# Performance work log

Measured on AMD Instinct MI355X. Metric: run time of the kernel, lower is better.

## Reference

```python
import jax, jax.numpy as jnp
import numpy as np

N_NODES = 100000
D_IN = 128
D_OUT = 128
SHAPES = {"r1": 1, "r2": 2, "r3": 3}
N_EDGES = {"r1": 400000, "r2": 300000, "r3": 200000}


def setup_inputs() -> dict:
    key = jax.random.key(0)
    ks = jax.random.split(key, 10)
    inp = {
        "x": jax.random.normal(ks[0], (N_NODES, D_IN), dtype=jnp.float32),
        "A_r1": jax.random.normal(ks[1], (D_IN * 1, D_OUT), dtype=jnp.float32) * 0.05,
        "A_r2": jax.random.normal(ks[2], (D_IN * 2, D_OUT), dtype=jnp.float32) * 0.05,
        "A_r3": jax.random.normal(ks[3], (D_IN * 3, D_OUT), dtype=jnp.float32) * 0.05,
        "C_w": jax.random.normal(ks[4], (D_IN, D_OUT), dtype=jnp.float32) * 0.05,
        "C_b": jax.random.normal(ks[5], (D_OUT,), dtype=jnp.float32) * 0.05,
    }
    for j, (name, shape) in enumerate(SHAPES.items()):
        n = N_EDGES[name] * shape
        inp[f"ei_{name}"] = jax.random.randint(ks[6 + j], (2, n), 0, N_NODES, dtype=jnp.int64)
    return inp


def _edge_type_agg(x, edge_indices, A, shape):
    # edge_indices: [2, n_edges*shape]; row0 = sources, row1 reshaped -> dest per hyperedge
    dest = edge_indices[1].reshape(-1, shape)[:, 0]          # [n_edges]
    gathered = x[edge_indices[0]].reshape(-1, shape * x.shape[1])  # [n_edges, shape*D_IN]
    msg = gathered @ A                                        # [n_edges, D_OUT]
    # 1/count(dest) normalization (torch.unique counts == per-type in-degree)
    deg = jax.ops.segment_sum(jnp.ones_like(dest, dtype=msg.dtype), dest, num_segments=x.shape[0])
    msg = msg / deg[dest][:, None]
    return jax.ops.segment_sum(msg, dest, num_segments=x.shape[0])  # scatter_add


def reference(x, ei_r1, ei_r2, ei_r3, A_r1, A_r2, A_r3, C_w, C_b):
    agg = (_edge_type_agg(x, ei_r1, A_r1, 1)
           + _edge_type_agg(x, ei_r2, A_r2, 2)
           + _edge_type_agg(x, ei_r3, A_r3, 3))
    return x @ C_w + C_b + agg
```

## Files before the change

### kernel.cpp

```cpp
#include <hip/hip_runtime.h>

#define N_NODES 100000
#define D 128
#define NND 12800000L

typedef unsigned short u16;
typedef short s16x8 __attribute__((ext_vector_type(8)));
typedef float f32x4 __attribute__((ext_vector_type(4)));


#define ENTS_OFF 2004160L
#define AT_OFF   15604224L
#define Y_OFF    15833600L

__device__ __forceinline__ u16 f2b(float f) {
    union { float f; unsigned u; } v; v.f = f;
    unsigned r = (v.u + 0x7FFFu + ((v.u >> 16) & 1u)) >> 16;
    return (u16)r;
}
__device__ __forceinline__ float blo(unsigned w) { return __uint_as_float(w << 16); }
__device__ __forceinline__ float bhi(unsigned w) { return __uint_as_float(w & 0xFFFF0000u); }


__global__ __launch_bounds__(256) void init_kernel(
    const float* __restrict__ A1, const float* __restrict__ A2,
    const float* __restrict__ A3, const float* __restrict__ Cw,
    u16* __restrict__ ATb, int* __restrict__ deg) {
    int b = blockIdx.x, t = threadIdx.x;
    if (b < 293) {
        int i0 = (b * 256 + t) * 4;
#pragma unroll
        for (int r = 0; r < 4; r++)
            if (i0 + r < 300000) deg[i0 + r] = 0;
        return;
    }
    int mb = b - 293;
    int m = mb >> 6;
    int idx = (mb & 63) * 256 + t;
    int n = idx >> 7, kk = idx & 127;
    const float* src; int srow;
    if (m == 0)      { src = A1; srow = kk; }
    else if (m < 3)  { src = A2; srow = (m - 1) * 128 + kk; }
    else if (m < 6)  { src = A3; srow = (m - 3) * 128 + kk; }
    else             { src = Cw; srow = kk; }
    ATb[m * 16384 + n * 128 + kk] = f2b(src[(long)srow * 128 + n]);
}


__global__ __launch_bounds__(256) void deg_all(
    const int* __restrict__ e1, const int* __restrict__ e2, const int* __restrict__ e3,
    int ne1, int ne2, int ne3, int* __restrict__ deg) {
    int g = blockIdx.x * 256 + threadIdx.x;
    if (g < ne1) {
        atomicAdd(&deg[e1[ne1 + g]], 1);
    } else if (g < ne1 + ne2) {
        int e = g - ne1;
        atomicAdd(&deg[N_NODES + e2[ne2 * 2 + e * 2]], 1);
    } else if (g < ne1 + ne2 + ne3) {
        int e = g - ne1 - ne2;
        atomicAdd(&deg[2 * N_NODES + e3[ne3 * 3 + e * 3]], 1);
    }
}

__device__ __forceinline__ int ucnt(const int* deg, int d) {
    return 1 + deg[d] + 2 * deg[N_NODES + d] + 3 * deg[2 * N_NODES + d];
}


__global__ __launch_bounds__(256) void scan_reduce_u(const int* __restrict__ deg,
                                                     int* __restrict__ bsums, int n) {
    __shared__ int s[256];
    int t = threadIdx.x;
    int base = blockIdx.x * 1024 + t * 4;
    int loc = 0;
#pragma unroll
    for (int r = 0; r < 4; r++) {
        int idx = base + r;
        if (idx < n) loc += ucnt(deg, idx);
    }
    s[t] = loc;
    for (int off = 128; off > 0; off >>= 1) {
        __syncthreads();
        if (t < off) s[t] += s[t + off];
    }
    if (t == 0) bsums[blockIdx.x] = s[0];
}

__global__ __launch_bounds__(512) void scan_tops(const int* __restrict__ bsums,
                                                 int* __restrict__ boffs,
                                                 int* __restrict__ offs, int nb, int n) {
    __shared__ int s[512];
    int t = threadIdx.x;
    int v = (t < nb) ? bsums[t] : 0;
    s[t] = v;
    for (int off = 1; off < 512; off <<= 1) {
        __syncthreads();
        int x = (t >= off) ? s[t - off] : 0;
        __syncthreads();
        s[t] += x;
    }
    if (t < nb) boffs[t] = s[t] - v;
    if (t == nb - 1) offs[n] = s[t];
}

__global__ __launch_bounds__(256) void scan_final_u(
    const int* __restrict__ deg, const int* __restrict__ boffs,
    int* __restrict__ offs, int* __restrict__ cursor, int2* __restrict__ ents, int n) {
    __shared__ int s[256];
    int t = threadIdx.x;
    int base = blockIdx.x * 1024 + t * 4;
    int v[4], p[4];
#pragma unroll
    for (int r = 0; r < 4; r++) {
        int idx = base + r;
        v[r] = (idx < n) ? ucnt(deg, idx) : 0;
    }
    p[0] = 0; p[1] = v[0]; p[2] = v[0] + v[1]; p[3] = v[0] + v[1] + v[2];
    int tsum = p[3] + v[3];
    s[t] = tsum;
    for (int off = 1; off < 256; off <<= 1) {
        __syncthreads();
        int x = (t >= off) ? s[t - off] : 0;
        __syncthreads();
        s[t] += x;
    }
    int texcl = s[t] - tsum + boffs[blockIdx.x];
#pragma unroll
    for (int r = 0; r < 4; r++) {
        int idx = base + r;
        if (idx < n) {
            int val = texcl + p[r];
            offs[idx] = val;
            cursor[idx] = val + 1;
            ents[val] = make_int2(6 * N_NODES + idx, __float_as_int(1.0f));
        }
    }
}


__global__ __launch_bounds__(256) void scatter_all(
    const int* __restrict__ e1, const int* __restrict__ e2, const int* __restrict__ e3,
    int ne1, int ne2, int ne3, const int* __restrict__ deg,
    int* __restrict__ cursor, int2* __restrict__ ents) {
    int g = blockIdx.x * 256 + threadIdx.x;
    if (g < ne1) {
        int dest = e1[ne1 + g];
        float sc = 1.0f / (float)deg[dest];
        int pos = atomicAdd(&cursor[dest], 1);
        ents[pos] = make_int2(e1[g], __float_as_int(sc));
    } else if (g < ne1 + ne2) {
        int e = g - ne1;
        int dest = e2[ne2 * 2 + e * 2];
        float sc = 1.0f / (float)deg[N_NODES + dest];
        int pos = atomicAdd(&cursor[dest], 2);
        ents[pos]     = make_int2(1 * N_NODES + e2[e * 2],     __float_as_int(sc));
        ents[pos + 1] = make_int2(2 * N_NODES + e2[e * 2 + 1], __float_as_int(sc));
    } else if (g < ne1 + ne2 + ne3) {
        int e = g - ne1 - ne2;
        int dest = e3[ne3 * 3 + e * 3];
        float sc = 1.0f / (float)deg[2 * N_NODES + dest];
        int pos = atomicAdd(&cursor[dest], 3);
#pragma unroll
        for (int s = 0; s < 3; s++)
            ents[pos + s] = make_int2((3 + s) * N_NODES + e3[e * 3 + s], __float_as_int(sc));
    }
}


__global__ __launch_bounds__(256) void gemm_all(
    const float* __restrict__ x, const u16* __restrict__ AT, u16* __restrict__ Y) {
    __shared__ float smemf[64 * 132];
    typedef u16 XsT[64][40];
    XsT* Xs = reinterpret_cast<XsT*>(smemf);

    const int t = threadIdx.x;
    const int d0 = blockIdx.x * 64;

#pragma unroll
    for (int i = 0; i < 8; i++) {
        int f = i * 256 + t;
        int row = f >> 5;
        int k4 = f & 31;
        int rs = d0 + row < N_NODES ? d0 + row : N_NODES - 1;
        float4 v = *(const float4*)&x[(long)rs * D + k4 * 4];
        int chunk = k4 >> 3, kk = (k4 & 7) * 4;
        u16* p = &Xs[chunk][row][kk];
        p[0] = f2b(v.x); p[1] = f2b(v.y); p[2] = f2b(v.z); p[3] = f2b(v.w);
    }
    __syncthreads();

    const int lane = t & 63, wv = t >> 6;
    const int nbase = wv * 32, quad = lane >> 4, lrow = lane & 15;

    s16x8 afrag[4][4];
#pragma unroll
    for (int mi = 0; mi < 4; mi++)
#pragma unroll
        for (int c = 0; c < 4; c++)
            afrag[mi][c] = *(const s16x8*)&Xs[c][mi * 16 + lrow][quad * 8];

    for (int w = 0; w < 7; w++) {
        const u16* B = AT + w * 16384;
        s16x8 bfrag[2][4];
#pragma unroll
        for (int ni = 0; ni < 2; ni++)
#pragma unroll
            for (int c = 0; c < 4; c++)
                bfrag[ni][c] = *(const s16x8*)(B + (long)(nbase + ni * 16 + lrow) * 128 +
                                               c * 32 + quad * 8);
        f32x4 acc[4][2];
#pragma unroll
        for (int mi = 0; mi < 4; mi++)
#pragma unroll
            for (int ni = 0; ni < 2; ni++) acc[mi][ni] = (f32x4)(0.0f);
#pragma unroll
        for (int c = 0; c < 4; c++)
#pragma unroll
            for (int mi = 0; mi < 4; mi++)
#pragma unroll
                for (int ni = 0; ni < 2; ni++)
                    acc[mi][ni] = __builtin_amdgcn_mfma_f32_16x16x32_bf16(
                        afrag[mi][c], bfrag[ni][c], acc[mi][ni], 0, 0, 0);

        __syncthreads();
#pragma unroll
        for (int mi = 0; mi < 4; mi++)
#pragma unroll
            for (int ni = 0; ni < 2; ni++)
#pragma unroll
                for (int reg = 0; reg < 4; reg++) {
                    int row = mi * 16 + quad * 4 + reg;
                    int col = nbase + ni * 16 + lrow;
                    smemf[row * 132 + col] = acc[mi][ni][reg];
                }
        __syncthreads();
        u16* Yw = Y + (long)w * NND;
#pragma unroll
        for (int i = 0; i < 8; i++) {
            int f = i * 256 + t;
            int row = f >> 5;
            int col = (f & 31) * 4;
            if (d0 + row < N_NODES) {
                float4 v = *(const float4*)&smemf[row * 132 + col];
                unsigned o0 = (unsigned)f2b(v.x) | ((unsigned)f2b(v.y) << 16);
                unsigned o1 = (unsigned)f2b(v.z) | ((unsigned)f2b(v.w) << 16);
                uint2 o = make_uint2(o0, o1);
                *(uint2*)(Yw + (long)(d0 + row) * D + col) = o;
            }
        }
        __syncthreads();
    }
}


__global__ __launch_bounds__(256) void gather_all(
    const u16* __restrict__ Y, const int2* __restrict__ ents,
    const int* __restrict__ offs, const float* __restrict__ Cb,
    float* __restrict__ out) {
    const int lane = threadIdx.x & 63;
    const int wv = __builtin_amdgcn_readfirstlane(threadIdx.x >> 6);
    int wid = blockIdx.x * 4 + wv;
    const int nw = gridDim.x * 4;
    const float cb0 = Cb[lane * 2];
    const float cb1 = Cb[lane * 2 + 1];

    for (int d = wid; d < N_NODES; d += nw) {
        int lo = offs[d];
        int hi = offs[d + 1];
        float a0 = 0.0f, a1 = 0.0f;
        for (int p = lo; p < hi; p += 8) {
            int2 e[8];
#pragma unroll
            for (int i = 0; i < 8; i++) {
                int q = p + i;
                e[i] = ents[q < hi ? q : hi - 1];
            }
            unsigned w[8];
#pragma unroll
            for (int i = 0; i < 8; i++)
                w[i] = *(const unsigned*)(Y + (long)e[i].x * D + lane * 2);
#pragma unroll
            for (int i = 0; i < 8; i++) {
                float s = (p + i < hi) ? __int_as_float(e[i].y) : 0.0f;
                a0 = fmaf(s, blo(w[i]), a0);
                a1 = fmaf(s, bhi(w[i]), a1);
            }
        }
        *(float2*)&out[(long)d * D + lane * 2] = make_float2(a0 + cb0, a1 + cb1);
    }
}


extern "C" void kernel_launch(void* const* d_in, const int* in_sizes, int n_in,
                              void* d_out, int out_size, void* d_ws, size_t ws_size,
                              hipStream_t stream) {
    const float* x  = (const float*)d_in[0];
    const float* A1 = (const float*)d_in[1];
    const float* A2 = (const float*)d_in[2];
    const float* A3 = (const float*)d_in[3];
    const float* Cw = (const float*)d_in[4];
    const float* Cb = (const float*)d_in[5];
    const int* e1 = (const int*)d_in[6];
    const int* e2 = (const int*)d_in[7];
    const int* e3 = (const int*)d_in[8];
    float* out = (float*)d_out;

    int* ws = (int*)d_ws;
    int* deg    = ws;
    int* offs   = ws + 300000;
    int* cursor = ws + 400001;
    int* bsums  = ws + 500001;
    int* boffs  = ws + 500513;
    int2* ents  = (int2*)((char*)d_ws + ENTS_OFF);
    u16* ATb    = (u16*)((char*)d_ws + AT_OFF);
    u16* Y      = (u16*)((char*)d_ws + Y_OFF);

    const int NE1 = in_sizes[6] / 2;
    const int NE2 = in_sizes[7] / (2 * 2);
    const int NE3 = in_sizes[8] / (2 * 3);
    const int NET = NE1 + NE2 + NE3;
    const int n = N_NODES;
    const int NB = (n + 1023) / 1024;

    init_kernel<<<293 + 448, 256, 0, stream>>>(A1, A2, A3, Cw, ATb, deg);
    deg_all<<<(NET + 255) / 256, 256, 0, stream>>>(e1, e2, e3, NE1, NE2, NE3, deg);
    scan_reduce_u<<<NB, 256, 0, stream>>>(deg, bsums, n);
    scan_tops<<<1, 512, 0, stream>>>(bsums, boffs, offs, NB, n);
    scan_final_u<<<NB, 256, 0, stream>>>(deg, boffs, offs, cursor, ents, n);
    scatter_all<<<(NET + 255) / 256, 256, 0, stream>>>(e1, e2, e3, NE1, NE2, NE3,
                                                       deg, cursor, ents);
    gemm_all<<<(N_NODES + 63) / 64, 256, 0, stream>>>(x, ATb, Y);
    gather_all<<<2048, 256, 0, stream>>>(Y, ents, offs, Cb, out);
}
```

Before: 354.8 us.

## Aggregate raw features before projection, then run a single fused GEMM

Uses linearity to swap the order of work: neighbour features are gathered and averaged per destination and per hyperedge slot into a 7x128 bf16 staging row per node, and a single GEMM then projects the concatenated row to the output and adds the bias. Before, seven 128-wide bf16 projections were written to global memory and gathered back. Edge entries shrink to plain source ints grouped by type and slot, and normalisation is done once per node instead of per edge. The cost is a larger K=896 GEMM that reloads its A tile from global memory for each slice, plus an extra 896-wide bf16 staging buffer.

```diff
diff --git a/kernel.cpp b/kernel.cpp
--- a/kernel.cpp
+++ b/kernel.cpp
@@ -2,30 +2,33 @@
 
 #define N_NODES 100000
 #define D 128
-#define NND 12800000L
 
 typedef unsigned short u16;
 typedef short s16x8 __attribute__((ext_vector_type(8)));
 typedef float f32x4 __attribute__((ext_vector_type(4)));
 
 
-#define ENTS_OFF 2004160L
-#define AT_OFF   15604224L
-#define Y_OFF    15833600L
+#define ENTS_OFF 2804224L
+#define AT_OFF   9204224L
+#define G_OFF    9433600L
 
 __device__ __forceinline__ u16 f2b(float f) {
     union { float f; unsigned u; } v; v.f = f;
     unsigned r = (v.u + 0x7FFFu + ((v.u >> 16) & 1u)) >> 16;
     return (u16)r;
 }
+__device__ __forceinline__ unsigned pk(float lo, float hi) {
+    return (unsigned)f2b(lo) | ((unsigned)f2b(hi) << 16);
+}
 __device__ __forceinline__ float blo(unsigned w) { return __uint_as_float(w << 16); }
 __device__ __forceinline__ float bhi(unsigned w) { return __uint_as_float(w & 0xFFFF0000u); }
 
 
 __global__ __launch_bounds__(256) void init_kernel(
+    const float* __restrict__ x,
     const float* __restrict__ A1, const float* __restrict__ A2,
     const float* __restrict__ A3, const float* __restrict__ Cw,
-    u16* __restrict__ ATb, int* __restrict__ deg) {
+    u16* __restrict__ ATb, u16* __restrict__ G, int* __restrict__ deg) {
     int b = blockIdx.x, t = threadIdx.x;
     if (b < 293) {
         int i0 = (b * 256 + t) * 4;
@@ -34,16 +37,28 @@
             if (i0 + r < 300000) deg[i0 + r] = 0;
         return;
     }
-    int mb = b - 293;
-    int m = mb >> 6;
-    int idx = (mb & 63) * 256 + t;
-    int n = idx >> 7, kk = idx & 127;
-    const float* src; int srow;
-    if (m == 0)      { src = A1; srow = kk; }
-    else if (m < 3)  { src = A2; srow = (m - 1) * 128 + kk; }
-    else if (m < 6)  { src = A3; srow = (m - 3) * 128 + kk; }
-    else             { src = Cw; srow = kk; }
-    ATb[m * 16384 + n * 128 + kk] = f2b(src[(long)srow * 128 + n]);
+    if (b < 741) {
+        int mb = b - 293;
+        int m = mb >> 6;
+        int idx = (mb & 63) * 256 + t;
+        int n = idx >> 7, kk = idx & 127;
+        const float* src; int srow;
+        if (m == 0)      { src = A1; srow = kk; }
+        else if (m < 3)  { src = A2; srow = (m - 1) * 128 + kk; }
+        else if (m < 6)  { src = A3; srow = (m - 3) * 128 + kk; }
+        else             { src = Cw; srow = kk; }
+        ATb[m * 16384 + n * 128 + kk] = f2b(src[(long)srow * 128 + n]);
+        return;
+    }
+    int f = (b - 741) * 256 + t;
+    int node = f >> 4, j = f & 15;
+    const float* xr = x + (long)node * 128 + j * 8;
+    float4 v0 = *(const float4*)xr;
+    float4 v1 = *(const float4*)(xr + 4);
+    uint4 o;
+    o.x = pk(v0.x, v0.y); o.y = pk(v0.z, v0.w);
+    o.z = pk(v1.x, v1.y); o.w = pk(v1.z, v1.w);
+    *(uint4*)(G + (long)node * 896 + 768 + j * 8) = o;
 }
 
 
@@ -63,7 +78,7 @@
 }
 
 __device__ __forceinline__ int ucnt(const int* deg, int d) {
-    return 1 + deg[d] + 2 * deg[N_NODES + d] + 3 * deg[2 * N_NODES + d];
+    return deg[d] + 2 * deg[N_NODES + d] + 3 * deg[2 * N_NODES + d];
 }
 
 
@@ -105,7 +120,7 @@
 
 __global__ __launch_bounds__(256) void scan_final_u(
     const int* __restrict__ deg, const int* __restrict__ boffs,
-    int* __restrict__ offs, int* __restrict__ cursor, int2* __restrict__ ents, int n) {
+    int* __restrict__ offs, int* __restrict__ cursor, int n) {
     __shared__ int s[256];
     int t = threadIdx.x;
     int base = blockIdx.x * 1024 + t * 4;
@@ -131,8 +146,10 @@
         if (idx < n) {
             int val = texcl + p[r];
             offs[idx] = val;
-            cursor[idx] = val + 1;
-            ents[val] = make_int2(6 * N_NODES + idx, __float_as_int(1.0f));
+            int c1 = deg[idx], c2 = deg[N_NODES + idx];
+            cursor[idx] = val;
+            cursor[N_NODES + idx] = val + c1;
+            cursor[2 * N_NODES + idx] = val + c1 + 2 * c2;
         }
     }
 }
@@ -141,152 +158,189 @@
 __global__ __launch_bounds__(256) void scatter_all(
     const int* __restrict__ e1, const int* __restrict__ e2, const int* __restrict__ e3,
     int ne1, int ne2, int ne3, const int* __restrict__ deg,
-    int* __restrict__ cursor, int2* __restrict__ ents) {
+    int* __restrict__ cursor, int* __restrict__ ents) {
     int g = blockIdx.x * 256 + threadIdx.x;
     if (g < ne1) {
         int dest = e1[ne1 + g];
-        float sc = 1.0f / (float)deg[dest];
         int pos = atomicAdd(&cursor[dest], 1);
-        ents[pos] = make_int2(e1[g], __float_as_int(sc));
+        ents[pos] = e1[g];
     } else if (g < ne1 + ne2) {
         int e = g - ne1;
         int dest = e2[ne2 * 2 + e * 2];
-        float sc = 1.0f / (float)deg[N_NODES + dest];
-        int pos = atomicAdd(&cursor[dest], 2);
-        ents[pos]     = make_int2(1 * N_NODES + e2[e * 2],     __float_as_int(sc));
-        ents[pos + 1] = make_int2(2 * N_NODES + e2[e * 2 + 1], __float_as_int(sc));
+        int c2 = deg[N_NODES + dest];
+        int pos = atomicAdd(&cursor[N_NODES + dest], 1);
+        ents[pos]      = e2[e * 2];
+        ents[pos + c2] = e2[e * 2 + 1];
     } else if (g < ne1 + ne2 + ne3) {
         int e = g - ne1 - ne2;
         int dest = e3[ne3 * 3 + e * 3];
-        float sc = 1.0f / (float)deg[2 * N_NODES + dest];
-        int pos = atomicAdd(&cursor[dest], 3);
-#pragma unroll
-        for (int s = 0; s < 3; s++)
-            ents[pos + s] = make_int2((3 + s) * N_NODES + e3[e * 3 + s], __float_as_int(sc));
-    }
-}
-
-
-__global__ __launch_bounds__(256) void gemm_all(
-    const float* __restrict__ x, const u16* __restrict__ AT, u16* __restrict__ Y) {
-    __shared__ float smemf[64 * 132];
+        int c3 = deg[2 * N_NODES + dest];
+        int pos = atomicAdd(&cursor[2 * N_NODES + dest], 1);
+        ents[pos]          = e3[e * 3];
+        ents[pos + c3]     = e3[e * 3 + 1];
+        ents[pos + 2 * c3] = e3[e * 3 + 2];
+    }
+}
+
+
+__global__ __launch_bounds__(256) void agg_all(
+    u16* __restrict__ G, const int* __restrict__ ents,
+    const int* __restrict__ offs, const int* __restrict__ deg) {
+    const int lane = threadIdx.x & 63;
+    const int wv = threadIdx.x >> 6;
+    int wid = blockIdx.x * 4 + wv;
+    const int nw = gridDim.x * 4;
+    const int col = lane * 2;
+
+    for (int d = wid; d < N_NODES; d += nw) {
+        const int lo = offs[d];
+        const int c1 = deg[d], c2 = deg[N_NODES + d], c3 = deg[2 * N_NODES + d];
+        float a0l = 0, a0h = 0, a1l = 0, a1h = 0, a2l = 0, a2h = 0;
+        float a3l = 0, a3h = 0, a4l = 0, a4h = 0, a5l = 0, a5h = 0;
+
+        for (int p = 0; p < c1; p += 4) {
+            unsigned w[4]; float m[4];
+#pragma unroll
+            for (int i = 0; i < 4; i++) {
+                int q = (p + i < c1) ? p + i : c1 - 1;
+                int src = ents[lo + q];
+                w[i] = *(const unsigned*)(G + (long)src * 896 + 768 + col);
+                m[i] = (p + i < c1) ? 1.0f : 0.0f;
+            }
+#pragma unroll
+            for (int i = 0; i < 4; i++) {
+                a0l = fmaf(m[i], blo(w[i]), a0l);
+                a0h = fmaf(m[i], bhi(w[i]), a0h);
+            }
+        }
+        const int o1 = lo + c1;
+        for (int p = 0; p < c2; p += 4) {
+            unsigned wa[4], wb[4]; float m[4];
+#pragma unroll
+            for (int i = 0; i < 4; i++) {
+                int q = (p + i < c2) ? p + i : c2 - 1;
+                int sa = ents[o1 + q];
+                int sb = ents[o1 + q + c2];
+                wa[i] = *(const unsigned*)(G + (long)sa * 896 + 768 + col);
+                wb[i] = *(const unsigned*)(G + (long)sb * 896 + 768 + col);
+                m[i] = (p + i < c2) ? 1.0f : 0.0f;
+            }
+#pragma unroll
+            for (int i = 0; i < 4; i++) {
+                a1l = fmaf(m[i], blo(wa[i]), a1l); a1h = fmaf(m[i], bhi(wa[i]), a1h);
+                a2l = fmaf(m[i], blo(wb[i]), a2l); a2h = fmaf(m[i], bhi(wb[i]), a2h);
+            }
+        }
+        const int o3 = o1 + 2 * c2;
+        for (int p = 0; p < c3; p += 4) {
+            unsigned wa[4], wb[4], wc[4]; float m[4];
+#pragma unroll
+            for (int i = 0; i < 4; i++) {
+                int q = (p + i < c3) ? p + i : c3 - 1;
+                int sa = ents[o3 + q];
+                int sb = ents[o3 + q + c3];
+                int sc = ents[o3 + q + 2 * c3];
+                wa[i] = *(const unsigned*)(G + (long)sa * 896 + 768 + col);
+                wb[i] = *(const unsigned*)(G + (long)sb * 896 + 768 + col);
+                wc[i] = *(const unsigned*)(G + (long)sc * 896 + 768 + col);
+                m[i] = (p + i < c3) ? 1.0f : 0.0f;
+            }
+#pragma unroll
+            for (int i = 0; i < 4; i++) {
+                a3l = fmaf(m[i], blo(wa[i]), a3l); a3h = fmaf(m[i], bhi(wa[i]), a3h);
+                a4l = fmaf(m[i], blo(wb[i]), a4l); a4h = fmaf(m[i], bhi(wb[i]), a4h);
+                a5l = fmaf(m[i], blo(wc[i]), a5l); a5h = fmaf(m[i], bhi(wc[i]), a5h);
+            }
+        }
+        const float i1 = c1 ? 1.0f / (float)c1 : 0.0f;
+        const float i2 = c2 ? 1.0f / (float)c2 : 0.0f;
+        const float i3 = c3 ? 1.0f / (float)c3 : 0.0f;
+        u16* gd = G + (long)d * 896 + col;
+        *(unsigned*)(gd)       = pk(a0l * i1, a0h * i1);
+        *(unsigned*)(gd + 128) = pk(a1l * i2, a1h * i2);
+        *(unsigned*)(gd + 256) = pk(a2l * i2, a2h * i2);
+        *(unsigned*)(gd + 384) = pk(a3l * i3, a3h * i3);
+        *(unsigned*)(gd + 512) = pk(a4l * i3, a4h * i3);
+        *(unsigned*)(gd + 640) = pk(a5l * i3, a5h * i3);
+    }
+}
+
+
+__global__ __launch_bounds__(256) void gemm_out(
+    const u16* __restrict__ G, const u16* __restrict__ AT,
+    const float* __restrict__ Cb, float* __restrict__ out) {
+    __shared__ __align__(16) float smemf[64 * 132];
     typedef u16 XsT[64][40];
     XsT* Xs = reinterpret_cast<XsT*>(smemf);
 
     const int t = threadIdx.x;
     const int d0 = blockIdx.x * 64;
-
+    const int lane = t & 63, wv = t >> 6;
+    const int nbase = wv * 32, quad = lane >> 4, lrow = lane & 15;
+
+    f32x4 acc[4][2];
+#pragma unroll
+    for (int mi = 0; mi < 4; mi++)
+#pragma unroll
+        for (int ni = 0; ni < 2; ni++) acc[mi][ni] = (f32x4)(0.0f);
+
+    for (int s = 0; s < 7; s++) {
+#pragma unroll
+        for (int i = 0; i < 4; i++) {
+            int f = i * 256 + t;
+            int row = f >> 4, k8 = f & 15;
+            long rs = (d0 + row < N_NODES) ? d0 + row : N_NODES - 1;
+            uint4 v = *(const uint4*)(G + rs * 896 + s * 128 + k8 * 8);
+            *(uint4*)&Xs[k8 >> 2][row][(k8 & 3) * 8] = v;
+        }
+        __syncthreads();
+        const u16* B = AT + s * 16384;
+        s16x8 bfrag[2][4];
+#pragma unroll
+        for (int ni = 0; ni < 2; ni++)
+#pragma unroll
+            for (int c = 0; c < 4; c++)
+                bfrag[ni][c] = *(const s16x8*)(B + (nbase + ni * 16 + lrow) * 128 +
+                                               c * 32 + quad * 8);
+        s16x8 afrag[4][4];
+#pragma unroll
+        for (int mi = 0; mi < 4; mi++)
+#pragma unroll
+            for (int c = 0; c < 4; c++)
+                afrag[mi][c] = *(const s16x8*)&Xs[c][mi * 16 + lrow][quad * 8];
+#pragma unroll
+        for (int c = 0; c < 4; c++)
+#pragma unroll
+            for (int mi = 0; mi < 4; mi++)
+#pragma unroll
+                for (int ni = 0; ni < 2; ni++)
+                    acc[mi][ni] = __builtin_amdgcn_mfma_f32_16x16x32_bf16(
+                        afrag[mi][c], bfrag[ni][c], acc[mi][ni], 0, 0, 0);
+        __syncthreads();
+    }
+
+#pragma unroll
+    for (int mi = 0; mi < 4; mi++)
+#pragma unroll
+        for (int ni = 0; ni < 2; ni++)
+#pragma unroll
+            for (int reg = 0; reg < 4; reg++) {
+                int row = mi * 16 + quad * 4 + reg;
+                int colq = nbase + ni * 16 + lrow;
+                smemf[row * 132 + colq] = acc[mi][ni][reg];
+            }
+    __syncthreads();
 #pragma unroll
     for (int i = 0; i < 8; i++) {
         int f = i * 256 + t;
         int row = f >> 5;
-        int k4 = f & 31;
-        int rs = d0 + row < N_NODES ? d0 + row : N_NODES - 1;
-        float4 v = *(const float4*)&x[(long)rs * D + k4 * 4];
-        int chunk = k4 >> 3, kk = (k4 & 7) * 4;
-        u16* p = &Xs[chunk][row][kk];
-        p[0] = f2b(v.x); p[1] = f2b(v.y); p[2] = f2b(v.z); p[3] = f2b(v.w);
-    }
-    __syncthreads();
-
-    const int lane = t & 63, wv = t >> 6;
-    const int nbase = wv * 32, quad = lane >> 4, lrow = lane & 15;
-
-    s16x8 afrag[4][4];
-#pragma unroll
-    for (int mi = 0; mi < 4; mi++)
-#pragma unroll
-        for (int c = 0; c < 4; c++)
-            afrag[mi][c] = *(const s16x8*)&Xs[c][mi * 16 + lrow][quad * 8];
-
-    for (int w = 0; w < 7; w++) {
-        const u16* B = AT + w * 16384;
-        s16x8 bfrag[2][4];
-#pragma unroll
-        for (int ni = 0; ni < 2; ni++)
-#pragma unroll
-            for (int c = 0; c < 4; c++)
-                bfrag[ni][c] = *(const s16x8*)(B + (long)(nbase + ni * 16 + lrow) * 128 +
-                                               c * 32 + quad * 8);
-        f32x4 acc[4][2];
-#pragma unroll
-        for (int mi = 0; mi < 4; mi++)
-#pragma unroll
-            for (int ni = 0; ni < 2; ni++) acc[mi][ni] = (f32x4)(0.0f);
-#pragma unroll
-        for (int c = 0; c < 4; c++)
-#pragma unroll
-            for (int mi = 0; mi < 4; mi++)
-#pragma unroll
-                for (int ni = 0; ni < 2; ni++)
-                    acc[mi][ni] = __builtin_amdgcn_mfma_f32_16x16x32_bf16(
-                        afrag[mi][c], bfrag[ni][c], acc[mi][ni], 0, 0, 0);
-
-        __syncthreads();
-#pragma unroll
-        for (int mi = 0; mi < 4; mi++)
-#pragma unroll
-            for (int ni = 0; ni < 2; ni++)
-#pragma unroll
-                for (int reg = 0; reg < 4; reg++) {
-                    int row = mi * 16 + quad * 4 + reg;
-                    int col = nbase + ni * 16 + lrow;
-                    smemf[row * 132 + col] = acc[mi][ni][reg];
-                }
-        __syncthreads();
-        u16* Yw = Y + (long)w * NND;
-#pragma unroll
-        for (int i = 0; i < 8; i++) {
-            int f = i * 256 + t;
-            int row = f >> 5;
-            int col = (f & 31) * 4;
-            if (d0 + row < N_NODES) {
-                float4 v = *(const float4*)&smemf[row * 132 + col];
-                unsigned o0 = (unsigned)f2b(v.x) | ((unsigned)f2b(v.y) << 16);
-                unsigned o1 = (unsigned)f2b(v.z) | ((unsigned)f2b(v.w) << 16);
-                uint2 o = make_uint2(o0, o1);
-                *(uint2*)(Yw + (long)(d0 + row) * D + col) = o;
-            }
-        }
-        __syncthreads();
-    }
-}
-
-
-__global__ __launch_bounds__(256) void gather_all(
-    const u16* __restrict__ Y, const int2* __restrict__ ents,
-    const int* __restrict__ offs, const float* __restrict__ Cb,
-    float* __restrict__ out) {
-    const int lane = threadIdx.x & 63;
-    const int wv = __builtin_amdgcn_readfirstlane(threadIdx.x >> 6);
-    int wid = blockIdx.x * 4 + wv;
-    const int nw = gridDim.x * 4;
-    const float cb0 = Cb[lane * 2];
-    const float cb1 = Cb[lane * 2 + 1];
-
-    for (int d = wid; d < N_NODES; d += nw) {
-        int lo = offs[d];
-        int hi = offs[d + 1];
-        float a0 = 0.0f, a1 = 0.0f;
-        for (int p = lo; p < hi; p += 8) {
-            int2 e[8];
-#pragma unroll
-            for (int i = 0; i < 8; i++) {
-                int q = p + i;
-                e[i] = ents[q < hi ? q : hi - 1];
-            }
-            unsigned w[8];
-#pragma unroll
-            for (int i = 0; i < 8; i++)
-                w[i] = *(const unsigned*)(Y + (long)e[i].x * D + lane * 2);
-#pragma unroll
-            for (int i = 0; i < 8; i++) {
-                float s = (p + i < hi) ? __int_as_float(e[i].y) : 0.0f;
-                a0 = fmaf(s, blo(w[i]), a0);
-                a1 = fmaf(s, bhi(w[i]), a1);
-            }
-        }
-        *(float2*)&out[(long)d * D + lane * 2] = make_float2(a0 + cb0, a1 + cb1);
+        int colq = (f & 31) * 4;
+        if (d0 + row < N_NODES) {
+            float4 v = *(const float4*)&smemf[row * 132 + colq];
+            float4 b = *(const float4*)&Cb[colq];
+            v.x += b.x; v.y += b.y; v.z += b.z; v.w += b.w;
+            *(float4*)&out[(long)(d0 + row) * 128 + colq] = v;
+        }
     }
 }
 
@@ -309,11 +363,11 @@
     int* deg    = ws;
     int* offs   = ws + 300000;
     int* cursor = ws + 400001;
-    int* bsums  = ws + 500001;
-    int* boffs  = ws + 500513;
-    int2* ents  = (int2*)((char*)d_ws + ENTS_OFF);
+    int* bsums  = ws + 700001;
+    int* boffs  = ws + 700513;
+    int* ents   = (int*)((char*)d_ws + ENTS_OFF);
     u16* ATb    = (u16*)((char*)d_ws + AT_OFF);
-    u16* Y      = (u16*)((char*)d_ws + Y_OFF);
+    u16* G      = (u16*)((char*)d_ws + G_OFF);
 
     const int NE1 = in_sizes[6] / 2;
     const int NE2 = in_sizes[7] / (2 * 2);
@@ -322,13 +376,13 @@
     const int n = N_NODES;
     const int NB = (n + 1023) / 1024;
 
-    init_kernel<<<293 + 448, 256, 0, stream>>>(A1, A2, A3, Cw, ATb, deg);
+    init_kernel<<<293 + 448 + 6250, 256, 0, stream>>>(x, A1, A2, A3, Cw, ATb, G, deg);
     deg_all<<<(NET + 255) / 256, 256, 0, stream>>>(e1, e2, e3, NE1, NE2, NE3, deg);
     scan_reduce_u<<<NB, 256, 0, stream>>>(deg, bsums, n);
     scan_tops<<<1, 512, 0, stream>>>(bsums, boffs, offs, NB, n);
-    scan_final_u<<<NB, 256, 0, stream>>>(deg, boffs, offs, cursor, ents, n);
+    scan_final_u<<<NB, 256, 0, stream>>>(deg, boffs, offs, cursor, n);
     scatter_all<<<(NET + 255) / 256, 256, 0, stream>>>(e1, e2, e3, NE1, NE2, NE3,
                                                        deg, cursor, ents);
-    gemm_all<<<(N_NODES + 63) / 64, 256, 0, stream>>>(x, ATb, Y);
-    gather_all<<<2048, 256, 0, stream>>>(Y, ents, offs, Cb, out);
-}
+    agg_all<<<2048, 256, 0, stream>>>(G, ents, offs, deg);
+    gemm_out<<<(N_NODES + 63) / 64, 256, 0, stream>>>(G, ATb, Cb, out);
+}
```

After: 364.5 us. 2.7% more time.
